# Kernel tuning notes

Hardware: AMD Instinct MI355X
Metric: run time of the kernel (lower is better)

## Reference

```python
import jax, jax.numpy as jnp
import numpy as np

N, E, D = 50000, 600000, 128
LN_EPS = 1e-5


def setup_inputs() -> dict:
    key = jax.random.key(0)
    ks = jax.random.split(key, 7)
    s = 1.0 / np.sqrt(D)
    x = jax.random.normal(ks[0], (N, D), dtype=jnp.float32)
    edge_index = jax.random.randint(ks[1], (2, E), 0, N, dtype=jnp.int32)
    Wq = jax.random.normal(ks[2], (D, D), dtype=jnp.float32) * s
    Wk = jax.random.normal(ks[3], (D, D), dtype=jnp.float32) * s
    Wv = jax.random.normal(ks[4], (D, D), dtype=jnp.float32) * s
    Wo = jax.random.normal(ks[5], (D, D), dtype=jnp.float32) * s
    bo = jnp.zeros((D,), dtype=jnp.float32)
    gamma = jnp.ones((D,), dtype=jnp.float32)
    beta = jnp.zeros((D,), dtype=jnp.float32)
    return {"x": x, "edge_index": edge_index, "Wq": Wq, "Wk": Wk,
            "Wv": Wv, "Wo": Wo, "bo": bo, "gamma": gamma, "beta": beta}


def reference(x, edge_index, Wq, Wk, Wv, Wo, bo, gamma, beta):
    src, dst = edge_index[0], edge_index[1]
    # gather endpoint features, project (torch Linear: y = x @ W.T)
    q = x[dst] @ Wq.T                      # [E, D]
    k = x[src] @ Wk.T                      # [E, D]
    v = x[src] @ Wv.T                      # [E, D]
    logits = jnp.sum(q * k, axis=-1, keepdims=True) / np.sqrt(D)  # [E, 1]
    msg = jax.nn.sigmoid(logits) * v       # [E, D]
    agg = jax.ops.segment_sum(msg, dst, num_segments=N)  # scatter-add -> [N, D]
    out = agg @ Wo.T + bo
    h = x + out
    # LayerNorm over last dim
    mu = jnp.mean(h, axis=-1, keepdims=True)
    var = jnp.mean(jnp.square(h - mu), axis=-1, keepdims=True)
    return (h - mu) * jax.lax.rsqrt(var + LN_EPS) * gamma + beta
```

## Files before the change

### kernel.cpp

```cpp
#include <hip/hip_runtime.h>
#include <math.h>


#define BM 64
#define NB 8

typedef __attribute__((ext_vector_type(8))) short bfrag;
typedef __attribute__((ext_vector_type(4))) float f32x4;

__device__ __forceinline__ short f2bf(float f) {
    union { float f; unsigned u; } v; v.f = f;
    unsigned r = v.u + 0x7FFFu + ((v.u >> 16) & 1u);
    return (short)(r >> 16);
}
__device__ __forceinline__ float bf2f(short h) {
    union { unsigned u; float f; } v;
    v.u = ((unsigned)(unsigned short)h) << 16;
    return v.f;
}
__device__ __forceinline__ float2 bfpair(unsigned w) {
    union { unsigned u; float f; } lo, hi;
    lo.u = w << 16;
    hi.u = w & 0xffff0000u;
    return make_float2(lo.f, hi.f);
}

__global__ __launch_bounds__(256) void zero_prep(
    const float* __restrict__ Wq, const float* __restrict__ Wk,
    const float* __restrict__ Wv, const float* __restrict__ Wo,
    short* __restrict__ whi, short* __restrict__ wlo,
    int* __restrict__ hist, int N)
{
    int g = blockIdx.x * 256 + threadIdx.x;
    if (g < N) hist[g] = 0;
    if (g < 65536) {
        const float* Ws[4] = {Wq, Wk, Wv, Wo};
        float f = Ws[g >> 14][g & 16383];
        short h = f2bf(f);
        short l = f2bf(f - bf2f(h));
        whi[g] = h; wlo[g] = l;
    }
}

__global__ __launch_bounds__(256) void qkv_mfma(
    const float* __restrict__ x,
    const short* __restrict__ whi, const short* __restrict__ wlo,
    float* __restrict__ Q, unsigned short* __restrict__ KV16, int N)
{
    __shared__ short xs_hi[64][136];
    __shared__ short xs_lo[64][136];

    const int tid = threadIdx.x;
    const int row0 = blockIdx.x * BM;

    #pragma unroll
    for (int i = 0; i < 8; ++i) {
        int idx = tid + 256 * i;
        int r = idx >> 5;
        int c4 = idx & 31;
        int gr = row0 + r;
        float4 val = make_float4(0.f, 0.f, 0.f, 0.f);
        if (gr < N) val = ((const float4*)(x + (size_t)gr * 128))[c4];
        short4 h, l;
        h.x = f2bf(val.x); l.x = f2bf(val.x - bf2f(h.x));
        h.y = f2bf(val.y); l.y = f2bf(val.y - bf2f(h.y));
        h.z = f2bf(val.z); l.z = f2bf(val.z - bf2f(h.z));
        h.w = f2bf(val.w); l.w = f2bf(val.w - bf2f(h.w));
        *((short4*)&xs_hi[r][c4 * 4]) = h;
        *((short4*)&xs_lo[r][c4 * 4]) = l;
    }
    __syncthreads();

    const int wid  = tid >> 6;
    const int lane = tid & 63;
    const int n16  = lane & 15;
    const int quad = lane >> 4;

    #pragma unroll 1
    for (int mat = 0; mat < 3; ++mat) {
        const short* __restrict__ WH = whi + mat * 16384;
        const short* __restrict__ WL = wlo + mat * 16384;
        const f32x4 zero = {0.f, 0.f, 0.f, 0.f};
        f32x4 acc[4][2];
        #pragma unroll
        for (int t = 0; t < 4; ++t) { acc[t][0] = zero; acc[t][1] = zero; }

        #pragma unroll
        for (int kc = 0; kc < 4; ++kc) {
            int k0 = kc * 32 + quad * 8;
            bfrag ah[4], al[4], bh[2], bl[2];
            #pragma unroll
            for (int t = 0; t < 4; ++t) {
                ah[t] = *((const bfrag*)&xs_hi[t * 16 + n16][k0]);
                al[t] = *((const bfrag*)&xs_lo[t * 16 + n16][k0]);
            }
            #pragma unroll
            for (int c = 0; c < 2; ++c) {
                int wr = (wid * 2 + c) * 16 + n16;
                bh[c] = *((const bfrag*)(WH + wr * 128 + k0));
                bl[c] = *((const bfrag*)(WL + wr * 128 + k0));
            }
            #pragma unroll
            for (int t = 0; t < 4; ++t)
                #pragma unroll
                for (int c = 0; c < 2; ++c) {
                    acc[t][c] = __builtin_amdgcn_mfma_f32_16x16x32_bf16(ah[t], bh[c], acc[t][c], 0, 0, 0);
                    acc[t][c] = __builtin_amdgcn_mfma_f32_16x16x32_bf16(al[t], bh[c], acc[t][c], 0, 0, 0);
                    acc[t][c] = __builtin_amdgcn_mfma_f32_16x16x32_bf16(ah[t], bl[c], acc[t][c], 0, 0, 0);
                }
        }
        #pragma unroll
        for (int t = 0; t < 4; ++t)
            #pragma unroll
            for (int r = 0; r < 4; ++r) {
                int grow = row0 + t * 16 + quad * 4 + r;
                if (grow < N) {
                    int c0 = (wid * 2 + 0) * 16 + n16;
                    int c1 = (wid * 2 + 1) * 16 + n16;
                    if (mat == 0) {
                        Q[(size_t)grow * 128 + c0] = acc[t][0][r];
                        Q[(size_t)grow * 128 + c1] = acc[t][1][r];
                    } else {
                        size_t base = (size_t)grow * 256 + (mat - 1);
                        KV16[base + 2 * c0] = (unsigned short)f2bf(acc[t][0][r]);
                        KV16[base + 2 * c1] = (unsigned short)f2bf(acc[t][1][r]);
                    }
                }
            }
    }
}

__global__ __launch_bounds__(256) void hist_kernel(
    const int* __restrict__ ei, int* __restrict__ hist, int E)
{
    int e = blockIdx.x * blockDim.x + threadIdx.x;
    if (e < E) atomicAdd(&hist[ei[E + e]], 1);
}

#define SCAN_TPB 256
#define SCAN_EPT 4

__global__ __launch_bounds__(SCAN_TPB) void scan_partial(
    const int* __restrict__ hist, int* __restrict__ offs,
    int* __restrict__ blockSums, int N)
{
    __shared__ int sdata[SCAN_TPB];
    int b = blockIdx.x;
    int t = threadIdx.x;
    int base = b * SCAN_TPB * SCAN_EPT + t * SCAN_EPT;
    int v[SCAN_EPT];
    int tot = 0;
    #pragma unroll
    for (int j = 0; j < SCAN_EPT; ++j) {
        int idx = base + j;
        v[j] = (idx < N) ? hist[idx] : 0;
        tot += v[j];
    }
    sdata[t] = tot;
    __syncthreads();
    for (int off = 1; off < SCAN_TPB; off <<= 1) {
        int xv = (t >= off) ? sdata[t - off] : 0;
        __syncthreads();
        sdata[t] += xv;
        __syncthreads();
    }
    int run = sdata[t] - tot;
    #pragma unroll
    for (int j = 0; j < SCAN_EPT; ++j) {
        int idx = base + j;
        if (idx < N) offs[idx] = run;
        run += v[j];
    }
    if (t == SCAN_TPB - 1) blockSums[b] = sdata[t];
}

__global__ __launch_bounds__(256) void scan_blocksums(int* __restrict__ blockSums, int nb)
{
    __shared__ int sdata[256];
    int t = threadIdx.x;
    int orig = (t < nb) ? blockSums[t] : 0;
    sdata[t] = orig;
    __syncthreads();
    for (int off = 1; off < 256; off <<= 1) {
        int xv = (t >= off) ? sdata[t - off] : 0;
        __syncthreads();
        sdata[t] += xv;
        __syncthreads();
    }
    if (t < nb) blockSums[t] = sdata[t] - orig;
}

__global__ __launch_bounds__(256) void scan_add(
    int* __restrict__ offs, int* __restrict__ starts,
    const int* __restrict__ blockSums, int N)
{
    int idx = blockIdx.x * blockDim.x + threadIdx.x;
    if (idx < N) {
        int vv = offs[idx] + blockSums[idx >> 10];
        offs[idx] = vv;
        starts[idx] = vv;
    }
}

__global__ __launch_bounds__(256) void scatter_kernel(
    const int* __restrict__ ei, int* __restrict__ offs,
    int* __restrict__ ssrc, int E)
{
    int e = blockIdx.x * blockDim.x + threadIdx.x;
    if (e < E) {
        int d = ei[E + e];
        int pos = atomicAdd(&offs[d], 1);
        ssrc[pos] = ei[e];
    }
}

__global__ __launch_bounds__(256) void node_agg(
    const int* __restrict__ ssrc,
    const int* __restrict__ starts,
    const int* __restrict__ endoffs,
    const float* __restrict__ Q, const unsigned short* __restrict__ KV16,
    float* __restrict__ agg, int N)
{
    int node = blockIdx.x * 4 + (threadIdx.x >> 6);
    int lane = threadIdx.x & 63;
    if (node >= N) return;
    int start = starts[node];
    int end = endoffs[node];
    float2 q = *((const float2*)(Q + (size_t)node * 128 + lane * 2));
    float a0 = 0.f, a1 = 0.f;

    for (int i = start; i < end; i += NB) {
        int s[NB];
        #pragma unroll
        for (int j = 0; j < NB; ++j) {
            int idx = i + j;
            idx = (idx < end) ? idx : (end - 1);
            s[j] = ssrc[idx];
        }
        uint2 w[NB];
        #pragma unroll
        for (int j = 0; j < NB; ++j)
            w[j] = *((const uint2*)(KV16 + (size_t)s[j] * 256 + lane * 4));
        float p[NB];
        #pragma unroll
        for (int j = 0; j < NB; ++j) {
            float2 kv0 = bfpair(w[j].x);
            float2 kv1 = bfpair(w[j].y);
            p[j] = q.x * kv0.x + q.y * kv1.x;
        }
        #pragma unroll
        for (int j = 0; j < NB; ++j)
            p[j] += __int_as_float(__builtin_amdgcn_ds_swizzle(__float_as_int(p[j]), 0x041F));
        #pragma unroll
        for (int j = 0; j < NB; ++j)
            p[j] += __int_as_float(__builtin_amdgcn_ds_swizzle(__float_as_int(p[j]), 0x081F));
        #pragma unroll
        for (int j = 0; j < NB; ++j)
            p[j] += __int_as_float(__builtin_amdgcn_ds_swizzle(__float_as_int(p[j]), 0x101F));
        #pragma unroll
        for (int j = 0; j < NB; ++j)
            p[j] += __int_as_float(__builtin_amdgcn_ds_swizzle(__float_as_int(p[j]), 0x201F));
        #pragma unroll
        for (int j = 0; j < NB; ++j)
            p[j] += __int_as_float(__builtin_amdgcn_ds_swizzle(__float_as_int(p[j]), 0x401F));
        #pragma unroll
        for (int j = 0; j < NB; ++j)
            p[j] += __shfl_xor(p[j], 32);

        #pragma unroll
        for (int j = 0; j < NB; ++j) {
            float c = 1.f / (1.f + __expf(-p[j] * 0.0883883476483184f));
            if (i + j >= end) c = 0.f;
            float2 kv0 = bfpair(w[j].x);
            float2 kv1 = bfpair(w[j].y);
            a0 += c * kv0.y; a1 += c * kv1.y;
        }
    }
    *((float2*)(agg + (size_t)node * 128 + lane * 2)) = make_float2(a0, a1);
}

__global__ __launch_bounds__(256) void out_ln_mfma(
    const float* __restrict__ agg,
    const short* __restrict__ whi, const short* __restrict__ wlo,
    const float* __restrict__ bo, const float* __restrict__ x,
    const float* __restrict__ gamma, const float* __restrict__ beta,
    float* __restrict__ out, int N)
{
    __shared__ __align__(16) char smem[64 * 136 * 2 * 2];
    short (*xs_hi)[136] = (short(*)[136])smem;
    short (*xs_lo)[136] = (short(*)[136])(smem + 64 * 136 * 2);
    float (*hs)[132]    = (float(*)[132])smem;

    const int tid = threadIdx.x;
    const int row0 = blockIdx.x * BM;

    #pragma unroll
    for (int i = 0; i < 8; ++i) {
        int idx = tid + 256 * i;
        int r = idx >> 5;
        int c4 = idx & 31;
        int gr = row0 + r;
        float4 val = make_float4(0.f, 0.f, 0.f, 0.f);
        if (gr < N) val = ((const float4*)(agg + (size_t)gr * 128))[c4];
        short4 h, l;
        h.x = f2bf(val.x); l.x = f2bf(val.x - bf2f(h.x));
        h.y = f2bf(val.y); l.y = f2bf(val.y - bf2f(h.y));
        h.z = f2bf(val.z); l.z = f2bf(val.z - bf2f(h.z));
        h.w = f2bf(val.w); l.w = f2bf(val.w - bf2f(h.w));
        *((short4*)&xs_hi[r][c4 * 4]) = h;
        *((short4*)&xs_lo[r][c4 * 4]) = l;
    }
    __syncthreads();

    const int wid  = tid >> 6;
    const int lane = tid & 63;
    const int n16  = lane & 15;
    const int quad = lane >> 4;
    const short* __restrict__ WH = whi + 3 * 16384;
    const short* __restrict__ WL = wlo + 3 * 16384;

    const f32x4 zero = {0.f, 0.f, 0.f, 0.f};
    f32x4 acc[4][2];
    #pragma unroll
    for (int t = 0; t < 4; ++t) { acc[t][0] = zero; acc[t][1] = zero; }

    #pragma unroll
    for (int kc = 0; kc < 4; ++kc) {
        int k0 = kc * 32 + quad * 8;
        bfrag ah[4], al[4], bh[2], bl[2];
        #pragma unroll
        for (int t = 0; t < 4; ++t) {
            ah[t] = *((const bfrag*)&xs_hi[t * 16 + n16][k0]);
            al[t] = *((const bfrag*)&xs_lo[t * 16 + n16][k0]);
        }
        #pragma unroll
        for (int c = 0; c < 2; ++c) {
            int wr = (wid * 2 + c) * 16 + n16;
            bh[c] = *((const bfrag*)(WH + wr * 128 + k0));
            bl[c] = *((const bfrag*)(WL + wr * 128 + k0));
        }
        #pragma unroll
        for (int t = 0; t < 4; ++t)
            #pragma unroll
            for (int c = 0; c < 2; ++c) {
                acc[t][c] = __builtin_amdgcn_mfma_f32_16x16x32_bf16(ah[t], bh[c], acc[t][c], 0, 0, 0);
                acc[t][c] = __builtin_amdgcn_mfma_f32_16x16x32_bf16(al[t], bh[c], acc[t][c], 0, 0, 0);
                acc[t][c] = __builtin_amdgcn_mfma_f32_16x16x32_bf16(ah[t], bl[c], acc[t][c], 0, 0, 0);
            }
    }
    __syncthreads();

    #pragma unroll
    for (int t = 0; t < 4; ++t)
        #pragma unroll
        for (int r = 0; r < 4; ++r) {
            hs[t * 16 + quad * 4 + r][(wid * 2 + 0) * 16 + n16] = acc[t][0][r];
            hs[t * 16 + quad * 4 + r][(wid * 2 + 1) * 16 + n16] = acc[t][1][r];
        }
    __syncthreads();

    {
        int r = tid >> 2;
        int qd = tid & 3;
        int gr = row0 + r;
        float sum = 0.f, sq = 0.f;
        #pragma unroll
        for (int c = 0; c < 32; c += 4) {
            float4 g4 = *((float4*)&hs[r][qd * 32 + c]);
            float4 b4 = *((const float4*)(bo + qd * 32 + c));
            float4 x4 = make_float4(0.f, 0.f, 0.f, 0.f);
            if (gr < N) x4 = *((const float4*)(x + (size_t)gr * 128 + qd * 32 + c));
            float4 h = make_float4(g4.x + b4.x + x4.x, g4.y + b4.y + x4.y,
                                   g4.z + b4.z + x4.z, g4.w + b4.w + x4.w);
            *((float4*)&hs[r][qd * 32 + c]) = h;
            sum += h.x + h.y + h.z + h.w;
            sq += h.x * h.x + h.y * h.y + h.z * h.z + h.w * h.w;
        }
        sum += __shfl_xor(sum, 1); sum += __shfl_xor(sum, 2);
        sq  += __shfl_xor(sq, 1);  sq  += __shfl_xor(sq, 2);
        float mu = sum * (1.f / 128.f);
        float var = sq * (1.f / 128.f) - mu * mu;
        float rs = rsqrtf(var + 1e-5f);
        if (gr < N) {
            #pragma unroll
            for (int c = 0; c < 32; c += 4) {
                float4 h = *((float4*)&hs[r][qd * 32 + c]);
                float4 g = *((const float4*)(gamma + qd * 32 + c));
                float4 b = *((const float4*)(beta + qd * 32 + c));
                float4 o = make_float4((h.x - mu) * rs * g.x + b.x,
                                       (h.y - mu) * rs * g.y + b.y,
                                       (h.z - mu) * rs * g.z + b.z,
                                       (h.w - mu) * rs * g.w + b.w);
                *((float4*)(out + (size_t)gr * 128 + qd * 32 + c)) = o;
            }
        }
    }
}

extern "C" void kernel_launch(void* const* d_in, const int* in_sizes, int n_in,
                              void* d_out, int out_size, void* d_ws, size_t ws_size,
                              hipStream_t stream) {
    const float* x     = (const float*)d_in[0];
    const int*   ei    = (const int*)d_in[1];
    const float* Wq    = (const float*)d_in[2];
    const float* Wk    = (const float*)d_in[3];
    const float* Wv    = (const float*)d_in[4];
    const float* Wo    = (const float*)d_in[5];
    const float* bo    = (const float*)d_in[6];
    const float* gamma = (const float*)d_in[7];
    const float* beta  = (const float*)d_in[8];
    const int N = in_sizes[0] / 128;
    const int E = in_sizes[1] / 2;
    const size_t ND = (size_t)N * 128;

    float* ws  = (float*)d_ws;
    float* Q   = ws;
    unsigned short* KV16 = (unsigned short*)(Q + ND);
    float* agg = (float*)(KV16 + 2 * ND);
    int* hist      = (int*)(agg + ND);
    int* offs      = hist + N;
    int* starts    = offs + N;
    int* blockSums = starts + N;
    int* ssrc      = blockSums + 256;
    short* whi     = (short*)(ssrc + E);
    short* wlo     = whi + 4 * 16384;

    const int gzp = ((N > 65536 ? N : 65536) + 255) / 256;
    zero_prep<<<gzp, 256, 0, stream>>>(Wq, Wk, Wv, Wo, whi, wlo, hist, N);

    hist_kernel<<<(E + 255) / 256, 256, 0, stream>>>(ei, hist, E);
    const int nScanBlocks = (N + SCAN_TPB * SCAN_EPT - 1) / (SCAN_TPB * SCAN_EPT);
    scan_partial<<<nScanBlocks, SCAN_TPB, 0, stream>>>(hist, offs, blockSums, N);
    scan_blocksums<<<1, 256, 0, stream>>>(blockSums, nScanBlocks);
    scan_add<<<(N + 255) / 256, 256, 0, stream>>>(offs, starts, blockSums, N);
    scatter_kernel<<<(E + 255) / 256, 256, 0, stream>>>(ei, offs, ssrc, E);

    const int gq = (N + BM - 1) / BM;
    qkv_mfma<<<gq, 256, 0, stream>>>(x, whi, wlo, Q, KV16, N);

    node_agg<<<(N + 3) / 4, 256, 0, stream>>>(ssrc, starts, offs, Q, KV16, agg, N);

    out_ln_mfma<<<gq, 256, 0, stream>>>(agg, whi, wlo, bo, x, gamma, beta,
                                        (float*)d_out, N);
}
```

Before: 276.6 us.

## Split node edges across half-waves with fp16 Q/KV and packed dot2

Q is now stored in fp16 instead of fp32, and K/V are stored in fp16 in a 4+4 interleaved layout, so each lane does one 16-byte load per edge. In node_agg, each half-wave handles half of a node's edge list, and the two halves are combined with a single cross-half shuffle at the end. The q·k dot uses v_dot2 fp16 instructions. This is meant to cut Q traffic, widen the per-lane loads and double in-flight edges per wave. The trade is fp16 range and precision in place of bf16/fp32, and a smaller unroll depth (4).

```diff
diff --git a/kernel.cpp b/kernel.cpp
--- a/kernel.cpp
+++ b/kernel.cpp
@@ -3,10 +3,10 @@
 
 
 #define BM 64
-#define NB 8
 
 typedef __attribute__((ext_vector_type(8))) short bfrag;
 typedef __attribute__((ext_vector_type(4))) float f32x4;
+typedef __attribute__((ext_vector_type(2))) _Float16 half2_t;
 
 __device__ __forceinline__ short f2bf(float f) {
     union { float f; unsigned u; } v; v.f = f;
@@ -18,11 +18,15 @@
     v.u = ((unsigned)(unsigned short)h) << 16;
     return v.f;
 }
-__device__ __forceinline__ float2 bfpair(unsigned w) {
-    union { unsigned u; float f; } lo, hi;
-    lo.u = w << 16;
-    hi.u = w & 0xffff0000u;
-    return make_float2(lo.f, hi.f);
+__device__ __forceinline__ unsigned short f2h(float f) {
+    union { _Float16 h; unsigned short u; } v;
+    v.h = (_Float16)f;
+    return v.u;
+}
+__device__ __forceinline__ half2_t u2h2(unsigned u) {
+    union { unsigned u; half2_t h; } v;
+    v.u = u;
+    return v.h;
 }
 
 __global__ __launch_bounds__(256) void zero_prep(
@@ -45,7 +49,7 @@
 __global__ __launch_bounds__(256) void qkv_mfma(
     const float* __restrict__ x,
     const short* __restrict__ whi, const short* __restrict__ wlo,
-    float* __restrict__ Q, unsigned short* __restrict__ KV16, int N)
+    unsigned short* __restrict__ Qh, unsigned short* __restrict__ KV16, int N)
 {
     __shared__ short xs_hi[64][136];
     __shared__ short xs_lo[64][136];
@@ -118,12 +122,13 @@
                     int c0 = (wid * 2 + 0) * 16 + n16;
                     int c1 = (wid * 2 + 1) * 16 + n16;
                     if (mat == 0) {
-                        Q[(size_t)grow * 128 + c0] = acc[t][0][r];
-                        Q[(size_t)grow * 128 + c1] = acc[t][1][r];
+                        Qh[(size_t)grow * 128 + c0] = f2h(acc[t][0][r]);
+                        Qh[(size_t)grow * 128 + c1] = f2h(acc[t][1][r]);
                     } else {
-                        size_t base = (size_t)grow * 256 + (mat - 1);
-                        KV16[base + 2 * c0] = (unsigned short)f2bf(acc[t][0][r]);
-                        KV16[base + 2 * c1] = (unsigned short)f2bf(acc[t][1][r]);
+                        int off = (mat == 2) ? 4 : 0;
+                        size_t base = (size_t)grow * 256;
+                        KV16[base + (c0 >> 2) * 8 + (c0 & 3) + off] = f2h(acc[t][0][r]);
+                        KV16[base + (c1 >> 2) * 8 + (c1 & 3) + off] = f2h(acc[t][1][r]);
                     }
                 }
             }
@@ -214,69 +219,85 @@
     }
 }
 
+#define NA 4
 __global__ __launch_bounds__(256) void node_agg(
     const int* __restrict__ ssrc,
     const int* __restrict__ starts,
     const int* __restrict__ endoffs,
-    const float* __restrict__ Q, const unsigned short* __restrict__ KV16,
+    const unsigned short* __restrict__ Qh,
+    const unsigned short* __restrict__ KV16,
     float* __restrict__ agg, int N)
 {
     int node = blockIdx.x * 4 + (threadIdx.x >> 6);
     int lane = threadIdx.x & 63;
     if (node >= N) return;
+    int half = lane >> 5;
+    int l = lane & 31;
+
     int start = starts[node];
     int end = endoffs[node];
-    float2 q = *((const float2*)(Q + (size_t)node * 128 + lane * 2));
-    float a0 = 0.f, a1 = 0.f;
-
-    for (int i = start; i < end; i += NB) {
-        int s[NB];
-        #pragma unroll
-        for (int j = 0; j < NB; ++j) {
-            int idx = i + j;
-            idx = (idx < end) ? idx : (end - 1);
+    int deg = end - start;
+    int len0 = (deg + 1) >> 1;
+    int hstart = start + half * len0;
+    int hend = half ? end : (start + len0);
+
+    uint2 qw = *((const uint2*)(Qh + (size_t)node * 128 + l * 4));
+    half2_t q01 = u2h2(qw.x), q23 = u2h2(qw.y);
+
+    float a0 = 0.f, a1 = 0.f, a2 = 0.f, a3 = 0.f;
+    int iters = (len0 + NA - 1) / NA;
+
+    int base = hstart;
+    for (int it = 0; it < iters; ++it, base += NA) {
+        int s[NA]; bool ok[NA];
+        #pragma unroll
+        for (int j = 0; j < NA; ++j) {
+            int idx = base + j;
+            ok[j] = (idx < hend);
+            idx = ok[j] ? idx : (hend - 1);
             s[j] = ssrc[idx];
         }
-        uint2 w[NB];
-        #pragma unroll
-        for (int j = 0; j < NB; ++j)
-            w[j] = *((const uint2*)(KV16 + (size_t)s[j] * 256 + lane * 4));
-        float p[NB];
-        #pragma unroll
-        for (int j = 0; j < NB; ++j) {
-            float2 kv0 = bfpair(w[j].x);
-            float2 kv1 = bfpair(w[j].y);
-            p[j] = q.x * kv0.x + q.y * kv1.x;
-        }
-        #pragma unroll
-        for (int j = 0; j < NB; ++j)
+        uint4 w[NA];
+        #pragma unroll
+        for (int j = 0; j < NA; ++j)
+            w[j] = *((const uint4*)(KV16 + (size_t)s[j] * 256 + l * 8));
+        float p[NA];
+        #pragma unroll
+        for (int j = 0; j < NA; ++j) {
+            p[j] = __builtin_amdgcn_fdot2(u2h2(w[j].x), q01, 0.f, false);
+            p[j] = __builtin_amdgcn_fdot2(u2h2(w[j].y), q23, p[j], false);
+        }
+        #pragma unroll
+        for (int j = 0; j < NA; ++j)
             p[j] += __int_as_float(__builtin_amdgcn_ds_swizzle(__float_as_int(p[j]), 0x041F));
         #pragma unroll
-        for (int j = 0; j < NB; ++j)
+        for (int j = 0; j < NA; ++j)
             p[j] += __int_as_float(__builtin_amdgcn_ds_swizzle(__float_as_int(p[j]), 0x081F));
         #pragma unroll
-        for (int j = 0; j < NB; ++j)
+        for (int j = 0; j < NA; ++j)
             p[j] += __int_as_float(__builtin_amdgcn_ds_swizzle(__float_as_int(p[j]), 0x101F));
         #pragma unroll
-        for (int j = 0; j < NB; ++j)
+        for (int j = 0; j < NA; ++j)
             p[j] += __int_as_float(__builtin_amdgcn_ds_swizzle(__float_as_int(p[j]), 0x201F));
         #pragma unroll
-        for (int j = 0; j < NB; ++j)
+        for (int j = 0; j < NA; ++j)
             p[j] += __int_as_float(__builtin_amdgcn_ds_swizzle(__float_as_int(p[j]), 0x401F));
-        #pragma unroll
-        for (int j = 0; j < NB; ++j)
-            p[j] += __shfl_xor(p[j], 32);
-
-        #pragma unroll
-        for (int j = 0; j < NB; ++j) {
+
+        #pragma unroll
+        for (int j = 0; j < NA; ++j) {
             float c = 1.f / (1.f + __expf(-p[j] * 0.0883883476483184f));
-            if (i + j >= end) c = 0.f;
-            float2 kv0 = bfpair(w[j].x);
-            float2 kv1 = bfpair(w[j].y);
-            a0 += c * kv0.y; a1 += c * kv1.y;
-        }
-    }
-    *((float2*)(agg + (size_t)node * 128 + lane * 2)) = make_float2(a0, a1);
+            if (!ok[j]) c = 0.f;
+            half2_t v01 = u2h2(w[j].z), v23 = u2h2(w[j].w);
+            a0 += c * (float)v01.x; a1 += c * (float)v01.y;
+            a2 += c * (float)v23.x; a3 += c * (float)v23.y;
+        }
+    }
+    a0 += __shfl_xor(a0, 32);
+    a1 += __shfl_xor(a1, 32);
+    a2 += __shfl_xor(a2, 32);
+    a3 += __shfl_xor(a3, 32);
+    if (half == 0)
+        *((float4*)(agg + (size_t)node * 128 + l * 4)) = make_float4(a0, a1, a2, a3);
 }
 
 __global__ __launch_bounds__(256) void out_ln_mfma(
@@ -413,9 +434,8 @@
     const int E = in_sizes[1] / 2;
     const size_t ND = (size_t)N * 128;
 
-    float* ws  = (float*)d_ws;
-    float* Q   = ws;
-    unsigned short* KV16 = (unsigned short*)(Q + ND);
+    unsigned short* Qh   = (unsigned short*)d_ws;
+    unsigned short* KV16 = Qh + ND;
     float* agg = (float*)(KV16 + 2 * ND);
     int* hist      = (int*)(agg + ND);
     int* offs      = hist + N;
@@ -436,9 +456,9 @@
     scatter_kernel<<<(E + 255) / 256, 256, 0, stream>>>(ei, offs, ssrc, E);
 
     const int gq = (N + BM - 1) / BM;
-    qkv_mfma<<<gq, 256, 0, stream>>>(x, whi, wlo, Q, KV16, N);
-
-    node_agg<<<(N + 3) / 4, 256, 0, stream>>>(ssrc, starts, offs, Q, KV16, agg, N);
+    qkv_mfma<<<gq, 256, 0, stream>>>(x, whi, wlo, Qh, KV16, N);
+
+    node_agg<<<(N + 3) / 4, 256, 0, stream>>>(ssrc, starts, offs, Qh, KV16, agg, N);
 
     out_ln_mfma<<<gq, 256, 0, stream>>>(agg, whi, wlo, bo, x, gamma, beta,
                                         (float*)d_out, N);
```

Measured after the change: 283.7 us. +2.6%, slower.
